# Kernel tuning notes

Hardware: AMD Instinct MI355X
Metric: run time of the kernel (lower is better)

## Reference

```python
import jax, jax.numpy as jnp
import numpy as np
from jax import lax

B, T, D, H, O, L = 128, 2048, 64, 128, 32, 2


def _rnn_layer(x, lengths, W_ih, W_hh, b_ih, b_hh):
    """One tanh RNN layer over padded [B,T,*] input with packed semantics:
    hidden state is frozen at steps t >= lengths[b] (those steps do not exist
    in the packed sequence). Returns per-step hidden states [B,T,H]."""
    Bl, Tl, _ = x.shape
    Hl = W_hh.shape[0]
    # precompute input projection once: [B,T,H]
    x_proj = jnp.einsum('btd,hd->bth', x, W_ih) + b_ih + b_hh

    def step(h, inp):
        xp, t = inp  # xp: [B,H], t: scalar
        h_new = jnp.tanh(xp + h @ W_hh.T)
        h = jnp.where((t < lengths)[:, None], h_new, h)
        return h, h

    h0 = jnp.zeros((Bl, Hl), dtype=x.dtype)
    _, ys = lax.scan(step, h0, (x_proj.transpose(1, 0, 2), jnp.arange(Tl)))
    return ys.transpose(1, 0, 2)  # [B,T,H]


def setup_inputs() -> dict:
    key = jax.random.key(0)
    ks = jax.random.split(key, 12)
    x = jax.random.normal(ks[0], (B, T, D), dtype=jnp.float32)
    # descending-sorted lengths in [1, T] (pack_padded_sequence enforce_sorted)
    lengths = jnp.sort(jax.random.randint(ks[1], (B,), 1, T + 1).astype(jnp.int32))[::-1]
    s_in = 1.0 / np.sqrt(H)
    W_ih0 = jax.random.uniform(ks[2], (H, D), minval=-s_in, maxval=s_in)
    W_hh0 = jax.random.uniform(ks[3], (H, H), minval=-s_in, maxval=s_in)
    b_ih0 = jax.random.uniform(ks[4], (H,), minval=-s_in, maxval=s_in)
    b_hh0 = jax.random.uniform(ks[5], (H,), minval=-s_in, maxval=s_in)
    W_ih1 = jax.random.uniform(ks[6], (H, H), minval=-s_in, maxval=s_in)
    W_hh1 = jax.random.uniform(ks[7], (H, H), minval=-s_in, maxval=s_in)
    b_ih1 = jax.random.uniform(ks[8], (H,), minval=-s_in, maxval=s_in)
    b_hh1 = jax.random.uniform(ks[9], (H,), minval=-s_in, maxval=s_in)
    W_fc = jax.random.uniform(ks[10], (O, H), minval=-s_in, maxval=s_in)
    b_fc = jax.random.uniform(ks[11], (O,), minval=-s_in, maxval=s_in)
    return {"x": x, "lengths": lengths,
            "W_ih0": W_ih0, "W_hh0": W_hh0, "b_ih0": b_ih0, "b_hh0": b_hh0,
            "W_ih1": W_ih1, "W_hh1": W_hh1, "b_ih1": b_ih1, "b_hh1": b_hh1,
            "W_fc": W_fc, "b_fc": b_fc}


def reference(x, lengths, W_ih0, W_hh0, b_ih0, b_hh0,
              W_ih1, W_hh1, b_ih1, b_hh1, W_fc, b_fc):
    h1 = _rnn_layer(x, lengths, W_ih0, W_hh0, b_ih0, b_hh0)   # [B,T,H]
    h2 = _rnn_layer(h1, lengths, W_ih1, W_hh1, b_ih1, b_hh1)  # [B,T,H]
    # pad_packed_sequence zero-fills positions t >= length
    mask = (jnp.arange(T)[None, :] < lengths[:, None])[..., None]
    out = jnp.where(mask, h2, 0.0)
    # fc is applied to the zero-padded tensor (padded rows become b_fc)
    return jnp.einsum('bth,oh->bto', out, W_fc) + b_fc
```

## Files before the change

kernel.cpp:

```cpp
#include <hip/hip_runtime.h>

#define BB 128
#define TT 2048
#define DD 64
#define HH 128
#define OO 32
#define NB 16
#define SCALE 2.885390081777927f

typedef _Float16 f16x8 __attribute__((ext_vector_type(8)));
typedef __fp16   pk16x2 __attribute__((ext_vector_type(2)));
typedef float    f32x4 __attribute__((ext_vector_type(4)));

#define MFMA16(a,b,c) __builtin_amdgcn_mfma_f32_16x16x32_f16((a),(b),(c),0,0,0)

__device__ __forceinline__ f32x4 load4(const float* p){ return *(const f32x4*)p; }

__device__ __forceinline__ f16x8 afrag_s(const float* p, float s){
    float4 a = *(const float4*)p, b = *(const float4*)(p+4);
    f16x8 r;
    r[0]=(_Float16)(a.x*s); r[1]=(_Float16)(a.y*s); r[2]=(_Float16)(a.z*s); r[3]=(_Float16)(a.w*s);
    r[4]=(_Float16)(b.x*s); r[5]=(_Float16)(b.y*s); r[6]=(_Float16)(b.z*s); r[7]=(_Float16)(b.w*s);
    return r;
}

__device__ __forceinline__ float tanh_pre(float z){
#if __has_builtin(__builtin_amdgcn_exp2f)
    float e = __builtin_amdgcn_exp2f(z);
#else
    float e = exp2f(z);
#endif
    return __builtin_fmaf(-2.f, __builtin_amdgcn_rcpf(1.f + e), 1.f);
}

__device__ __forceinline__ unsigned pk2(float a, float b){
    union { pk16x2 h; unsigned u; } c;
    c.h = __builtin_amdgcn_cvt_pkrtz(a, b);
    return c.u;
}

__device__ __forceinline__ f16x8 xfrag(float4 a, float4 b){
    union { unsigned u[4]; f16x8 v; } c;
    c.u[0] = pk2(a.x, a.y); c.u[1] = pk2(a.z, a.w);
    c.u[2] = pk2(b.x, b.y); c.u[3] = pk2(b.z, b.w);
    return c.v;
}

#define LSTR2 136
#define PHB   (NB*LSTR2*2)

#define STEP_L1(T_, P_, XS_) do {                                             \
    const int t_ = (T_);                                                      \
    f16x8 bh1[4];                                                             \
    _Pragma("unroll")                                                         \
    for (int kt = 0; kt < 4; ++kt)                                            \
        bh1[kt] = *(const f16x8*)(h1b + (P_)*PHB + kt*64);                    \
    const bool doZ0 = (t_ < maxlen);                                          \
    f32x4 za[2], zb[2];                                                       \
    if (doZ0){                                                                \
        f16x8 xB0 = xfrag(XS_[0], XS_[1]);                                    \
        f16x8 xB1 = xfrag(XS_[2], XS_[3]);                                    \
        _Pragma("unroll")                                                     \
        for (int m = 0; m < 2; ++m){                                          \
            za[m] = bv0[m];                                                   \
            za[m] = MFMA16(Aih[m][0], xB0, za[m]);                            \
            zb[m][0]=0.f; zb[m][1]=0.f; zb[m][2]=0.f; zb[m][3]=0.f;           \
            zb[m] = MFMA16(Aih[m][1], xB1, zb[m]);                            \
        }                                                                     \
        _Pragma("unroll")                                                     \
        for (int m = 0; m < 2; ++m){                                          \
            za[m] = MFMA16(A0[m][0], bh1[0], za[m]);                          \
            zb[m] = MFMA16(A0[m][1], bh1[1], zb[m]);                          \
            za[m] = MFMA16(A0[m][2], bh1[2], za[m]);                          \
            zb[m] = MFMA16(A0[m][3], bh1[3], zb[m]);                          \
        }                                                                     \
    }                                                                         \
    {           \
        const int tl = (t_ + 2 < TT) ? (t_ + 2) : (TT - 1);                   \
        const float* xq = xb + (size_t)tl*DD;                                 \
        XS_[0] = *(const float4*)(xq);                                        \
        XS_[1] = *(const float4*)(xq + 4);                                    \
        XS_[2] = *(const float4*)(xq + 32);                                   \
        XS_[3] = *(const float4*)(xq + 36);                                   \
    }                                                                         \
    if (doZ0){                                                                \
        _Pragma("unroll")                                                     \
        for (int m = 0; m < 2; ++m){                                          \
            f32x4 zz = za[m] + zb[m];                                         \
            uint2 v;                                                          \
            v.x = pk2(tanh_pre(zz[0]), tanh_pre(zz[1]));                      \
            v.y = pk2(tanh_pre(zz[2]), tanh_pre(zz[3]));                      \
            *(uint2*)((char*)H1T + ((P_)^1)*PHB + n*272 + (w*2+m)*32 + q*8) = v; \
        }                                                                     \
    }                                                                         \
    asm volatile("s_waitcnt lgkmcnt(0)\n\ts_barrier" ::: "memory");           \
} while (0)

#define STEP_L2(T_, P_) do {                                                  \
    const int t_ = (T_);                                                      \
    f16x8 bh1[4], bh2[4];                                                     \
    _Pragma("unroll")                                                         \
    for (int kt = 0; kt < 4; ++kt){                                           \
        bh1[kt] = *(const f16x8*)(h1b + (P_)*PHB + kt*64);                    \
        bh2[kt] = *(const f16x8*)(h2b + (P_)*PHB + kt*64);                    \
    }                                                                         \
    const bool doZ1 = (t_ >= 1) && (t_ <= maxlen);                            \
    f32x4 za[2], zb[2], ya[2], yb[2];                                         \
    __builtin_amdgcn_s_setprio(1);                                            \
    if (doZ1){                                                                \
        _Pragma("unroll")                                                     \
        for (int m = 0; m < 2; ++m){                                          \
            za[m] = b1v[m];                                                   \
            zb[m][0]=0.f; zb[m][1]=0.f; zb[m][2]=0.f; zb[m][3]=0.f;           \
            ya[m] = zb[m]; yb[m] = zb[m];                                     \
        }                                                                     \
        _Pragma("unroll")                                                     \
        for (int m = 0; m < 2; ++m){                                          \
            za[m] = MFMA16(Ai[m][0], bh1[0], za[m]);                          \
            zb[m] = MFMA16(Ai[m][1], bh1[1], zb[m]);                          \
            ya[m] = MFMA16(Ah[m][0], bh2[0], ya[m]);                          \
            yb[m] = MFMA16(Ah[m][1], bh2[1], yb[m]);                          \
            za[m] = MFMA16(Ai[m][2], bh1[2], za[m]);                          \
            zb[m] = MFMA16(Ai[m][3], bh1[3], zb[m]);                          \
            ya[m] = MFMA16(Ah[m][2], bh2[2], ya[m]);                          \
            yb[m] = MFMA16(Ah[m][3], bh2[3], yb[m]);                          \
        }                                                                     \
    }                                                                         \
    if (doFC && t_ >= 2){                                                     \
        f32x4 zfa = bfv, zfb;                                                 \
        zfb[0]=0.f; zfb[1]=0.f; zfb[2]=0.f; zfb[3]=0.f;                       \
        zfa = MFMA16(Af[0], bh2[0], zfa);                                     \
        zfb = MFMA16(Af[1], bh2[1], zfb);                                     \
        zfa = MFMA16(Af[2], bh2[2], zfa);                                     \
        zfb = MFMA16(Af[3], bh2[3], zfb);                                     \
        if (t_ - 2 < lenn){                                                   \
            f32x4 zf = zfa + zfb;                                             \
            float4 sv; sv.x=zf[0]; sv.y=zf[1]; sv.z=zf[2]; sv.w=zf[3];        \
            *(float4*)(obase + (size_t)(t_-2)*OO) = sv;                       \
        }                                                                     \
    }                                                                         \
    __builtin_amdgcn_s_setprio(0);                                            \
    if (doZ1){                                                                \
        _Pragma("unroll")                                                     \
        for (int m = 0; m < 2; ++m){                                          \
            f32x4 zz = (za[m] + zb[m]) + (ya[m] + yb[m]);                     \
            uint2 v;                                                          \
            v.x = pk2(tanh_pre(zz[0]), tanh_pre(zz[1]));                      \
            v.y = pk2(tanh_pre(zz[2]), tanh_pre(zz[3]));                      \
            *(uint2*)((char*)H2T + ((P_)^1)*PHB + n*272 + (wl*2+m)*32 + q*8) = v; \
        }                                                                     \
    }                                                                         \
    asm volatile("s_waitcnt lgkmcnt(0)\n\ts_barrier" ::: "memory");           \
} while (0)

extern "C" __global__ void __launch_bounds__(512, 1)
scan_kernel(const float* __restrict__ x, const int* __restrict__ lengths,
            const float* __restrict__ W_ih0, const float* __restrict__ W_hh0,
            const float* __restrict__ b_ih0, const float* __restrict__ b_hh0,
            const float* __restrict__ W_ih1, const float* __restrict__ W_hh1,
            const float* __restrict__ b_ih1, const float* __restrict__ b_hh1,
            const float* __restrict__ W_fc,  const float* __restrict__ b_fc,
            float* __restrict__ out)
{
    const int tid  = threadIdx.x;
    const int w    = tid >> 6, lane = tid & 63;
    const int n    = lane & 15, q = lane >> 4;
    const int rbase= blockIdx.x * NB;

    __shared__ __align__(16) _Float16 H1T[2][NB][LSTR2];
    __shared__ __align__(16) _Float16 H2T[2][NB][LSTR2];

    for (int idx = tid; idx < (2*NB*LSTR2)/2; idx += 512){
        ((unsigned*)H1T)[idx] = 0u;
        ((unsigned*)H2T)[idx] = 0u;
    }

    const int lenn = lengths[rbase + n];
    int mx = lenn;
    #pragma unroll
    for (int s = 1; s < 16; s <<= 1){ int o = __shfl_xor(mx, s, 64); mx = max(mx, o); }
    const int maxlen = __builtin_amdgcn_readfirstlane(mx);

    const char* h1b = (const char*)H1T + n*272 + q*16;
    const char* h2b = (const char*)H2T + n*272 + q*16;

    __syncthreads();

    if (w < 4){
        f16x8 A0[2][4], Aih[2][2];
        f32x4 bv0[2];
        #pragma unroll
        for (int m = 0; m < 2; ++m){
            const int row = (w*2 + m)*16 + n;
            #pragma unroll
            for (int kt = 0; kt < 4; ++kt)
                A0[m][kt] = afrag_s(W_hh0 + row*HH + kt*32 + q*8, SCALE);
            #pragma unroll
            for (int kt = 0; kt < 2; ++kt)
                Aih[m][kt] = afrag_s(W_ih0 + row*DD + kt*32 + q*8, SCALE);
            bv0[m] = (load4(b_ih0 + (w*2+m)*16 + q*4)
                    + load4(b_hh0 + (w*2+m)*16 + q*4)) * SCALE;
        }

        const float* xb = x + ((size_t)(rbase+n)*TT)*DD + q*8;

        float4 xe[4], xo[4];
        {
            const float* x0 = xb;
            const float* x1 = xb + DD;
            xe[0] = *(const float4*)(x0);      xe[1] = *(const float4*)(x0 + 4);
            xe[2] = *(const float4*)(x0 + 32); xe[3] = *(const float4*)(x0 + 36);
            xo[0] = *(const float4*)(x1);      xo[1] = *(const float4*)(x1 + 4);
            xo[2] = *(const float4*)(x1 + 32); xo[3] = *(const float4*)(x1 + 36);
        }

        for (int t0 = 0; t0 <= maxlen + 1; t0 += 2){
            STEP_L1(t0,     0, xe);
            STEP_L1(t0 + 1, 1, xo);
        }
    } else {
        const int wl = w - 4;
        const bool doFC = (wl < 2);
        const int f = wl & 1;
        f16x8 Ai[2][4], Ah[2][4];
        f32x4 b1v[2];
        #pragma unroll
        for (int m = 0; m < 2; ++m){
            const int row = (wl*2 + m)*16 + n;
            #pragma unroll
            for (int kt = 0; kt < 4; ++kt){
                Ai[m][kt] = afrag_s(W_ih1 + row*HH + kt*32 + q*8, SCALE);
                Ah[m][kt] = afrag_s(W_hh1 + row*HH + kt*32 + q*8, SCALE);
            }
            b1v[m] = (load4(b_ih1 + (wl*2+m)*16 + q*4)
                    + load4(b_hh1 + (wl*2+m)*16 + q*4)) * SCALE;
        }
        f16x8 Af[4];
        #pragma unroll
        for (int kt = 0; kt < 4; ++kt)
            Af[kt] = afrag_s(W_fc + (f*16 + n)*HH + kt*32 + q*8, 1.0f);
        const f32x4 bfv = load4(b_fc + f*16 + q*4);

        float* obase = out + ((size_t)(rbase+n)*TT)*OO + f*16 + q*4;

        for (int t0 = 0; t0 <= maxlen + 1; t0 += 2){
            STEP_L2(t0,     0);
            STEP_L2(t0 + 1, 1);
        }
    }

    {
        const int row  = tid >> 5;
        const int lr   = lengths[rbase + row];
        const int o4   = tid & 7;
        const int tpar = (tid >> 3) & 3;
        const float4 bf4 = *(const float4*)(b_fc + o4*4);
        float* ob = out + ((size_t)(rbase+row)*TT)*OO + o4*4;
        for (int t = lr + tpar; t < TT; t += 4)
            *(float4*)(ob + (size_t)t*OO) = bf4;
    }
}

extern "C" void kernel_launch(void* const* d_in, const int* in_sizes, int n_in,
                              void* d_out, int out_size, void* d_ws, size_t ws_size,
                              hipStream_t stream)
{
    const float* x       = (const float*)d_in[0];
    const int*   lengths = (const int*)  d_in[1];
    const float* W_ih0   = (const float*)d_in[2];
    const float* W_hh0   = (const float*)d_in[3];
    const float* b_ih0   = (const float*)d_in[4];
    const float* b_hh0   = (const float*)d_in[5];
    const float* W_ih1   = (const float*)d_in[6];
    const float* W_hh1   = (const float*)d_in[7];
    const float* b_ih1   = (const float*)d_in[8];
    const float* b_hh1   = (const float*)d_in[9];
    const float* W_fc    = (const float*)d_in[10];
    const float* b_fc    = (const float*)d_in[11];

    scan_kernel<<<BB/NB, 512, 0, stream>>>(x, lengths, W_ih0, W_hh0,
                                           b_ih0, b_hh0,
                                           W_ih1, W_hh1, b_ih1, b_hh1,
                                           W_fc, b_fc, (float*)d_out);
}
```

Measured before the change: 1.584 ms.

## Deepen layer-1/layer-2 wavefront pipeline with 4-slot H1 ring and prefetched h1

The layer-1 hidden-state buffer becomes a 4-deep ring, and layer 2 lags layer 1 by one extra phase. Layer-2 waves now load their layer-1 input (rh1) at the end of the previous phase, before the barrier, so those LDS reads overlap the barrier wait instead of sitting on the critical path. The input-projection MFMAs then run on data already held in registers. This costs one extra pipeline phase, more shared memory and more registers, and the ring and phase indexing must be exactly right to stay correct.

```diff
diff --git a/kernel.cpp b/kernel.cpp
--- a/kernel.cpp
+++ b/kernel.cpp
@@ -49,13 +49,14 @@
 #define LSTR2 136
 #define PHB   (NB*LSTR2*2)
 
-#define STEP_L1(T_, P_, XS_) do {                                             \
-    const int t_ = (T_);                                                      \
+#define L1PHASE(P_, XS_) do {                                                 \
+    const int p_ = (P_);                                                      \
+    const char* rp = (const char*)H1R + ((p_+3)&3)*PHB + n*272 + q*16;        \
     f16x8 bh1[4];                                                             \
     _Pragma("unroll")                                                         \
     for (int kt = 0; kt < 4; ++kt)                                            \
-        bh1[kt] = *(const f16x8*)(h1b + (P_)*PHB + kt*64);                    \
-    const bool doZ0 = (t_ < maxlen);                                          \
+        bh1[kt] = *(const f16x8*)(rp + kt*64);                                \
+    const bool doZ0 = (p_ < maxlen);                                          \
     f32x4 za[2], zb[2];                                                       \
     if (doZ0){                                                                \
         f16x8 xB0 = xfrag(XS_[0], XS_[1]);                                    \
@@ -76,7 +77,7 @@
         }                                                                     \
     }                                                                         \
     {           \
-        const int tl = (t_ + 2 < TT) ? (t_ + 2) : (TT - 1);                   \
+        const int tl = (p_ + 2 < TT) ? (p_ + 2) : (TT - 1);                   \
         const float* xq = xb + (size_t)tl*DD;                                 \
         XS_[0] = *(const float4*)(xq);                                        \
         XS_[1] = *(const float4*)(xq + 4);                                    \
@@ -84,71 +85,82 @@
         XS_[3] = *(const float4*)(xq + 36);                                   \
     }                                                                         \
     if (doZ0){                                                                \
+        char* wp = (char*)H1R + (p_&3)*PHB + n*272 + (w*2)*32 + q*8;          \
         _Pragma("unroll")                                                     \
         for (int m = 0; m < 2; ++m){                                          \
             f32x4 zz = za[m] + zb[m];                                         \
             uint2 v;                                                          \
             v.x = pk2(tanh_pre(zz[0]), tanh_pre(zz[1]));                      \
             v.y = pk2(tanh_pre(zz[2]), tanh_pre(zz[3]));                      \
-            *(uint2*)((char*)H1T + ((P_)^1)*PHB + n*272 + (w*2+m)*32 + q*8) = v; \
+            *(uint2*)(wp + m*32) = v;                                         \
         }                                                                     \
     }                                                                         \
     asm volatile("s_waitcnt lgkmcnt(0)\n\ts_barrier" ::: "memory");           \
 } while (0)
 
-#define STEP_L2(T_, P_) do {                                                  \
-    const int t_ = (T_);                                                      \
-    f16x8 bh1[4], bh2[4];                                                     \
+#define L2PHASE(P_) do {                                                      \
+    const int p_ = (P_);                                                      \
+    const int u_ = p_ - 2;                                                    \
+        \
+    const char* rp2 = (const char*)H2P + ((p_+1)&1)*PHB + n*272 + q*16;       \
+    f16x8 bh2[4];                                                             \
     _Pragma("unroll")                                                         \
-    for (int kt = 0; kt < 4; ++kt){                                           \
-        bh1[kt] = *(const f16x8*)(h1b + (P_)*PHB + kt*64);                    \
-        bh2[kt] = *(const f16x8*)(h2b + (P_)*PHB + kt*64);                    \
-    }                                                                         \
-    const bool doZ1 = (t_ >= 1) && (t_ <= maxlen);                            \
+    for (int kt = 0; kt < 4; ++kt)                                            \
+        bh2[kt] = *(const f16x8*)(rp2 + kt*64);                               \
+    const bool doZ1 = (u_ >= 0) && (u_ < maxlen);                             \
     f32x4 za[2], zb[2], ya[2], yb[2];                                         \
     __builtin_amdgcn_s_setprio(1);                                            \
     if (doZ1){                                                                \
+          \
         _Pragma("unroll")                                                     \
         for (int m = 0; m < 2; ++m){                                          \
             za[m] = b1v[m];                                                   \
             zb[m][0]=0.f; zb[m][1]=0.f; zb[m][2]=0.f; zb[m][3]=0.f;           \
-            ya[m] = zb[m]; yb[m] = zb[m];                                     \
-        }                                                                     \
-        _Pragma("unroll")                                                     \
-        for (int m = 0; m < 2; ++m){                                          \
-            za[m] = MFMA16(Ai[m][0], bh1[0], za[m]);                          \
-            zb[m] = MFMA16(Ai[m][1], bh1[1], zb[m]);                          \
+            za[m] = MFMA16(Ai[m][0], rh1[0], za[m]);                          \
+            zb[m] = MFMA16(Ai[m][1], rh1[1], zb[m]);                          \
+            za[m] = MFMA16(Ai[m][2], rh1[2], za[m]);                          \
+            zb[m] = MFMA16(Ai[m][3], rh1[3], zb[m]);                          \
+        }                                                                     \
+        _Pragma("unroll")                                                     \
+        for (int m = 0; m < 2; ++m){                                          \
+            ya[m][0]=0.f; ya[m][1]=0.f; ya[m][2]=0.f; ya[m][3]=0.f;           \
+            yb[m] = ya[m];                                                    \
             ya[m] = MFMA16(Ah[m][0], bh2[0], ya[m]);                          \
             yb[m] = MFMA16(Ah[m][1], bh2[1], yb[m]);                          \
-            za[m] = MFMA16(Ai[m][2], bh1[2], za[m]);                          \
-            zb[m] = MFMA16(Ai[m][3], bh1[3], zb[m]);                          \
             ya[m] = MFMA16(Ah[m][2], bh2[2], ya[m]);                          \
             yb[m] = MFMA16(Ah[m][3], bh2[3], yb[m]);                          \
         }                                                                     \
     }                                                                         \
-    if (doFC && t_ >= 2){                                                     \
+    if (doFC && p_ >= 3){                                                     \
         f32x4 zfa = bfv, zfb;                                                 \
         zfb[0]=0.f; zfb[1]=0.f; zfb[2]=0.f; zfb[3]=0.f;                       \
         zfa = MFMA16(Af[0], bh2[0], zfa);                                     \
         zfb = MFMA16(Af[1], bh2[1], zfb);                                     \
         zfa = MFMA16(Af[2], bh2[2], zfa);                                     \
         zfb = MFMA16(Af[3], bh2[3], zfb);                                     \
-        if (t_ - 2 < lenn){                                                   \
+        if ((unsigned)(p_ - 3) < (unsigned)lenn){                             \
             f32x4 zf = zfa + zfb;                                             \
             float4 sv; sv.x=zf[0]; sv.y=zf[1]; sv.z=zf[2]; sv.w=zf[3];        \
-            *(float4*)(obase + (size_t)(t_-2)*OO) = sv;                       \
+            *(float4*)(obase + (size_t)(p_-3)*OO) = sv;                       \
         }                                                                     \
     }                                                                         \
     __builtin_amdgcn_s_setprio(0);                                            \
     if (doZ1){                                                                \
+        char* wp = (char*)H2P + (p_&1)*PHB + n*272 + (wl*2)*32 + q*8;         \
         _Pragma("unroll")                                                     \
         for (int m = 0; m < 2; ++m){                                          \
             f32x4 zz = (za[m] + zb[m]) + (ya[m] + yb[m]);                     \
             uint2 v;                                                          \
             v.x = pk2(tanh_pre(zz[0]), tanh_pre(zz[1]));                      \
             v.y = pk2(tanh_pre(zz[2]), tanh_pre(zz[3]));                      \
-            *(uint2*)((char*)H2T + ((P_)^1)*PHB + n*272 + (wl*2+m)*32 + q*8) = v; \
-        }                                                                     \
+            *(uint2*)(wp + m*32) = v;                                         \
+        }                                                                     \
+    }                                                                         \
+    {            \
+        const char* rh = (const char*)H1R + ((p_+3)&3)*PHB + n*272 + q*16;    \
+        _Pragma("unroll")                                                     \
+        for (int kt = 0; kt < 4; ++kt)                                        \
+            rh1[kt] = *(const f16x8*)(rh + kt*64);                            \
     }                                                                         \
     asm volatile("s_waitcnt lgkmcnt(0)\n\ts_barrier" ::: "memory");           \
 } while (0)
@@ -167,12 +179,12 @@
     const int n    = lane & 15, q = lane >> 4;
     const int rbase= blockIdx.x * NB;
 
-    __shared__ __align__(16) _Float16 H1T[2][NB][LSTR2];
-    __shared__ __align__(16) _Float16 H2T[2][NB][LSTR2];
-
-    for (int idx = tid; idx < (2*NB*LSTR2)/2; idx += 512){
-        ((unsigned*)H1T)[idx] = 0u;
-        ((unsigned*)H2T)[idx] = 0u;
+    __shared__ __align__(16) _Float16 H1R[4][NB][LSTR2];
+    __shared__ __align__(16) _Float16 H2P[2][NB][LSTR2];
+
+    for (int idx = tid; idx < (6*NB*LSTR2)/2; idx += 512){
+        if (idx < (4*NB*LSTR2)/2) ((unsigned*)H1R)[idx] = 0u;
+        else ((unsigned*)H2P)[idx - (4*NB*LSTR2)/2] = 0u;
     }
 
     const int lenn = lengths[rbase + n];
@@ -180,9 +192,6 @@
     #pragma unroll
     for (int s = 1; s < 16; s <<= 1){ int o = __shfl_xor(mx, s, 64); mx = max(mx, o); }
     const int maxlen = __builtin_amdgcn_readfirstlane(mx);
-
-    const char* h1b = (const char*)H1T + n*272 + q*16;
-    const char* h2b = (const char*)H2T + n*272 + q*16;
 
     __syncthreads();
 
@@ -214,9 +223,9 @@
             xo[2] = *(const float4*)(x1 + 32); xo[3] = *(const float4*)(x1 + 36);
         }
 
-        for (int t0 = 0; t0 <= maxlen + 1; t0 += 2){
-            STEP_L1(t0,     0, xe);
-            STEP_L1(t0 + 1, 1, xo);
+        for (int p0 = 0; p0 <= maxlen + 2; p0 += 2){
+            L1PHASE(p0,     xe);
+            L1PHASE(p0 + 1, xo);
         }
     } else {
         const int wl = w - 4;
@@ -243,9 +252,15 @@
 
         float* obase = out + ((size_t)(rbase+n)*TT)*OO + f*16 + q*4;
 
-        for (int t0 = 0; t0 <= maxlen + 1; t0 += 2){
-            STEP_L2(t0,     0);
-            STEP_L2(t0 + 1, 1);
+        f16x8 rh1[4];
+        #pragma unroll
+        for (int kt = 0; kt < 4; ++kt)
+            #pragma unroll
+            for (int j = 0; j < 8; ++j) rh1[kt][j] = (_Float16)0.f;
+
+        for (int p0 = 0; p0 <= maxlen + 2; p0 += 2){
+            L2PHASE(p0);
+            L2PHASE(p0 + 1);
         }
     }
 
```

Result: no change. 1.567 ms (-1.1%).
